# Kernel optimization log

Measured on AMD Instinct MI355X. Metric: run time of the kernel, lower is better.

Reference implementation:

```python
import jax, jax.numpy as jnp
import numpy as np

B, S, E, H, D = 4, 2048, 1024, 8, 128
EPS = 1e-5


def _ln(x, g, b):
    m = jnp.mean(x, axis=-1, keepdims=True)
    v = jnp.mean((x - m) ** 2, axis=-1, keepdims=True)
    return (x - m) * jax.lax.rsqrt(v + EPS) * g + b


def _xavier(k, shape, fan_in, fan_out):
    lim = float(np.sqrt(6.0 / (fan_in + fan_out)))
    return jax.random.uniform(k, shape, jnp.float32, -lim, lim)


def setup_inputs() -> dict:
    key = jax.random.key(0)
    ks = jax.random.split(key, 10)
    return {
        "x": jax.random.normal(ks[0], (B, S, E), jnp.float32),
        # embedding_to_z: Linear(E, H*D); stored as [E, H*D] for x @ W
        "W_ez": _xavier(ks[1], (E, H * D), E, H * D),
        "b_ez": jnp.zeros((H * D,), jnp.float32),
        "U_h": _xavier(ks[2], (H, D, D), D, D),
        "U_z": _xavier(ks[3], (H, D, D), D, D),
        "b_u": jnp.zeros((H, D), jnp.float32),
        "out_shaper": _xavier(ks[4], (H, D, D), D, D),
        # shared per-step state LayerNorm
        "lns_g": jnp.ones((D,), jnp.float32),
        "lns_b": jnp.zeros((D,), jnp.float32),
        # per-head FFN: LayerNorm(D) -> Linear(D,D) -> GELU -> Linear(D,E)
        "ff_ln_g": jnp.ones((H, D), jnp.float32),
        "ff_ln_b": jnp.zeros((H, D), jnp.float32),
        "ff_W1": _xavier(ks[5], (H, D, D), D, D),
        "ff_b1": jnp.zeros((H, D), jnp.float32),
        "ff_W2": _xavier(ks[6], (H, D, E), D, E),
        "ff_b2": jnp.zeros((H, E), jnp.float32),
        # layer_attention_weights: Linear(E, 1)
        "w_att": _xavier(ks[7], (E,), E, 1),
        "b_att": jnp.zeros((), jnp.float32),
        # output LayerNorm
        "lno_g": jnp.ones((E,), jnp.float32),
        "lno_b": jnp.zeros((E,), jnp.float32),
    }


def reference(x, W_ez, b_ez, U_h, U_z, b_u, out_shaper, lns_g, lns_b,
              ff_ln_g, ff_ln_b, ff_W1, ff_b1, ff_W2, ff_b2,
              w_att, b_att, lno_g, lno_b):
    b, s, _ = x.shape
    h, d = U_h.shape[0], U_h.shape[1]
    # z tokens: [B,S,H,D]
    z = jnp.tanh((x @ W_ez + b_ez).reshape(b, s, h, d))
    # torch.einsum('bhd,hdd->bhd') takes the DIAGONAL of the second operand
    uh_diag = jnp.einsum('hii->hi', U_h)          # [H,D]
    uz_diag = jnp.einsum('hii->hi', U_z)          # [H,D]
    os_diag = jnp.einsum('hii->hi', out_shaper)   # [H,D]

    def step(h_prev, z_t):
        # h_prev, z_t: [B,H,D]
        u = jax.nn.sigmoid(h_prev * uh_diag + z_t * uz_diag + b_u)
        h_new = u * h_prev + (1.0 - u) * z_t
        h_new = _ln(h_new, lns_g, lns_b)
        return h_new, h_new

    h0 = jnp.zeros((b, h, d), x.dtype)
    _, states = jax.lax.scan(step, h0, jnp.swapaxes(z, 0, 1))  # [S,B,H,D]
    states = jnp.swapaxes(states, 0, 1)                         # [B,S,H,D]

    shaped = states * os_diag                                   # diag einsum
    hln = _ln(shaped, ff_ln_g, ff_ln_b)                         # per-head LN
    h1 = jax.nn.gelu(jnp.einsum('bshd,hde->bshe', hln, ff_W1) + ff_b1,
                     approximate=False)                         # [B,S,H,D]
    ff_out = jnp.einsum('bshd,hde->bshe', h1, ff_W2) + ff_b2    # [B,S,H,E]

    scores = jax.nn.softmax(jnp.einsum('bshe,e->bsh', ff_out, w_att) + b_att,
                            axis=2)                             # over heads
    weighted = jnp.einsum('bshe,bsh->bse', ff_out, scores)      # [B,S,E]
    return _ln(weighted, lno_g, lno_b)
```

## Files before the change

### kernel.cpp

```cpp
#include <hip/hip_runtime.h>
#include <hip/hip_bf16.h>
#include <math.h>

#define BB 4
#define SS 2048
#define EE 1024
#define HH 8
#define DD 128
#define BSR (BB*SS)
#define HD  (HH*DD)
#define LNEPS 1e-5f
#define LOG2E 1.4426950408889634f

typedef __attribute__((ext_vector_type(8))) short bf16x8;
typedef __attribute__((ext_vector_type(4))) float f32x4;

__device__ __forceinline__ ushort f2bf(float f) {
    union { float f; unsigned u; } c{f};
    unsigned r = c.u + 0x7fff + ((c.u >> 16) & 1);
    return (ushort)(r >> 16);
}
__device__ __forceinline__ float bf2f(ushort b) {
    union { unsigned u; float f; } c{(unsigned)b << 16};
    return c.f;
}

typedef __attribute__((address_space(1))) const unsigned int GUI;
typedef __attribute__((address_space(3))) unsigned int LUI;
__device__ __forceinline__ void gl_lds16(const ushort* g, ushort* l) {
    __builtin_amdgcn_global_load_lds((GUI*)g, (LUI*)l, 16, 0, 0);
}

__device__ __forceinline__ float dpp_add(float x, const int ctrl) {
    int y;
    switch (ctrl) {
        case 0x111: y = __builtin_amdgcn_update_dpp(0, __float_as_int(x), 0x111, 0xf, 0xf, true); break;
        case 0x112: y = __builtin_amdgcn_update_dpp(0, __float_as_int(x), 0x112, 0xf, 0xf, true); break;
        case 0x114: y = __builtin_amdgcn_update_dpp(0, __float_as_int(x), 0x114, 0xf, 0xf, true); break;
        case 0x118: y = __builtin_amdgcn_update_dpp(0, __float_as_int(x), 0x118, 0xf, 0xf, true); break;
        case 0x142: y = __builtin_amdgcn_update_dpp(0, __float_as_int(x), 0x142, 0xf, 0xf, true); break;
        default:    y = __builtin_amdgcn_update_dpp(0, __float_as_int(x), 0x143, 0xf, 0xf, true); break;
    }
    return x + __int_as_float(y);
}

__device__ __forceinline__ float wave_sum64(float x) {
    x = dpp_add(x, 0x111);
    x = dpp_add(x, 0x112);
    x = dpp_add(x, 0x114);
    x = dpp_add(x, 0x118);
    x = dpp_add(x, 0x142);
    x = dpp_add(x, 0x143);
    return __int_as_float(__builtin_amdgcn_readlane(__float_as_int(x), 63));
}

__global__ __launch_bounds__(256)
void convx2_k(const float* __restrict__ x,
              ushort* __restrict__ hi, ushort* __restrict__ lo)
{
    const size_t idx = ((size_t)blockIdx.x * 256 + threadIdx.x) * 4;
    const float4 v = *(const float4*)(x + idx);
    ushort4 oh, ol;
    oh.x = f2bf(v.x); ol.x = f2bf(v.x - bf2f(oh.x));
    oh.y = f2bf(v.y); ol.y = f2bf(v.y - bf2f(oh.y));
    oh.z = f2bf(v.z); ol.z = f2bf(v.z - bf2f(oh.z));
    oh.w = f2bf(v.w); ol.w = f2bf(v.w - bf2f(oh.w));
    *(ushort4*)(hi + idx) = oh;
    *(ushort4*)(lo + idx) = ol;
}

__global__ __launch_bounds__(256)
void prepall_k(const float* __restrict__ W_ez,
               ushort* __restrict__ Wth, ushort* __restrict__ Wtl,
               const float* __restrict__ W2, ushort* __restrict__ W2t,
               const float* __restrict__ W1, ushort* __restrict__ W1t,
               const float* __restrict__ w_att, const float* __restrict__ b2,
               const float* __restrict__ b_att,
               const float* __restrict__ Uh, const float* __restrict__ Uz,
               const float* __restrict__ Os,
               float* __restrict__ q, float* __restrict__ c,
               float* __restrict__ uh_d, float* __restrict__ uz_d,
               float* __restrict__ os_d)
{
    __shared__ float tile[32][33];
    const int blk = blockIdx.x;
    const int tx = threadIdx.x & 31, ty = threadIdx.x >> 5;
    if (blk < 1024) {
        const int k0 = (blk >> 5) * 32, n0 = (blk & 31) * 32;
        #pragma unroll
        for (int i = 0; i < 4; ++i)
            tile[ty + i*8][tx] = W_ez[(size_t)(k0 + ty + i*8) * 1024 + n0 + tx];
        __syncthreads();
        #pragma unroll
        for (int i = 0; i < 4; ++i) {
            const float v = tile[tx][ty + i*8];
            const ushort h = f2bf(v);
            Wth[(size_t)(n0 + ty + i*8) * 1024 + k0 + tx] = h;
            Wtl[(size_t)(n0 + ty + i*8) * 1024 + k0 + tx] = f2bf(v - bf2f(h));
        }
    } else if (blk < 2048) {
        const int b2i = blk - 1024;
        const int k0 = (b2i >> 5) * 32, n0 = (b2i & 31) * 32;
        #pragma unroll
        for (int i = 0; i < 4; ++i)
            tile[ty + i*8][tx] = W2[(size_t)(k0 + ty + i*8) * 1024 + n0 + tx];
        __syncthreads();
        #pragma unroll
        for (int i = 0; i < 4; ++i)
            W2t[(size_t)(n0 + ty + i*8) * 1024 + k0 + tx] = f2bf(tile[tx][ty + i*8]);
    } else if (blk < 2176) {
        const int idx = blk - 2048;
        const int hh = idx >> 4;
        const int k0 = (idx & 3) * 32, n0 = ((idx >> 2) & 3) * 32;
        const float* Wb = W1 + (size_t)hh * DD * DD;
        ushort*      Wtb = W1t + (size_t)hh * DD * DD;
        #pragma unroll
        for (int i = 0; i < 4; ++i)
            tile[ty + i*8][tx] = Wb[(size_t)(k0 + ty + i*8) * DD + n0 + tx];
        __syncthreads();
        #pragma unroll
        for (int i = 0; i < 4; ++i)
            Wtb[(size_t)(n0 + ty + i*8) * DD + k0 + tx] = f2bf(tile[tx][ty + i*8]);
    } else {
        const int gid  = (blk - 2176) * 256 + threadIdx.x;
        const int wave = gid >> 6, lane = gid & 63;
        if (wave < HD) {
            const float* wp = W2 + (size_t)wave * EE;
            float p = 0.f;
            for (int e = lane; e < EE; e += 64) p = fmaf(wp[e], w_att[e], p);
            #pragma unroll
            for (int off = 32; off > 0; off >>= 1) p += __shfl_xor(p, off, 64);
            if (lane == 0) {
                q[wave] = p;
                const int h = wave >> 7, d = wave & 127;
                uh_d[wave] = Uh[(size_t)h*DD*DD + (size_t)d*DD + d];
                uz_d[wave] = Uz[(size_t)h*DD*DD + (size_t)d*DD + d];
                os_d[wave] = Os[(size_t)h*DD*DD + (size_t)d*DD + d];
            }
        } else if (wave < HD + HH) {
            const int h = wave - HD;
            const float* bp = b2 + (size_t)h * EE;
            float p = 0.f;
            for (int e = lane; e < EE; e += 64) p = fmaf(bp[e], w_att[e], p);
            #pragma unroll
            for (int off = 32; off > 0; off >>= 1) p += __shfl_xor(p, off, 64);
            if (lane == 0) c[h] = p + b_att[0];
        }
    }
}

__global__ __launch_bounds__(256)
void gemm_mfma_hp(const ushort* __restrict__ Ah, const ushort* __restrict__ Al,
                  const ushort* __restrict__ Bh, const ushort* __restrict__ Bl,
                  float* __restrict__ C, const float* __restrict__ bias)
{
    __shared__ ushort AsmH[128*32], AsmL[128*32];
    __shared__ ushort BsmH[128*32], BsmL[128*32];
    const int t = threadIdx.x, lane = t & 63, w = t >> 6;
    const int wr = w >> 1, wc = w & 1;
    const int row0 = blockIdx.x * 128, col0 = blockIdx.y * 128;

    const int lr = lane >> 2;
    const int lc = (lane & 3) ^ (lr & 3);
    const size_t aoff0 = (size_t)(row0 +      w*16 + lr) * 1024 + lc*8;
    const size_t aoff1 = (size_t)(row0 + 64 + w*16 + lr) * 1024 + lc*8;
    const size_t boff0 = (size_t)(col0 +      w*16 + lr) * 1024 + lc*8;
    const size_t boff1 = (size_t)(col0 + 64 + w*16 + lr) * 1024 + lc*8;
    ushort* AH0 = AsmH + (     w*16) * 32;  ushort* AH1 = AsmH + (64 + w*16) * 32;
    ushort* AL0 = AsmL + (     w*16) * 32;  ushort* AL1 = AsmL + (64 + w*16) * 32;
    ushort* BH0 = BsmH + (     w*16) * 32;  ushort* BH1 = BsmH + (64 + w*16) * 32;
    ushort* BL0 = BsmL + (     w*16) * 32;  ushort* BL1 = BsmL + (64 + w*16) * 32;

    f32x4 acc[4][4];
    #pragma unroll
    for (int i = 0; i < 4; ++i)
        #pragma unroll
        for (int j = 0; j < 4; ++j) acc[i][j] = (f32x4){0.f,0.f,0.f,0.f};

    const int quad = lane >> 4;
    const int fr   = lane & 15;
    const int fchk = (quad ^ (lane & 3)) * 8;

    for (int k0 = 0; k0 < 1024; k0 += 32) {
        __syncthreads();
        gl_lds16(Ah + aoff0 + k0, AH0);
        gl_lds16(Ah + aoff1 + k0, AH1);
        gl_lds16(Bh + boff0 + k0, BH0);
        gl_lds16(Bh + boff1 + k0, BH1);
        gl_lds16(Al + aoff0 + k0, AL0);
        gl_lds16(Al + aoff1 + k0, AL1);
        gl_lds16(Bl + boff0 + k0, BL0);
        gl_lds16(Bl + boff1 + k0, BL1);
        __syncthreads();

        bf16x8 afh[4], afl[4], bfh[4], bfl[4];
        #pragma unroll
        for (int i = 0; i < 4; ++i) {
            const int ra = (wr*64 + i*16 + fr) * 32 + fchk;
            afh[i] = *(const bf16x8*)(AsmH + ra);
            afl[i] = *(const bf16x8*)(AsmL + ra);
            const int rb = (wc*64 + i*16 + fr) * 32 + fchk;
            bfh[i] = *(const bf16x8*)(BsmH + rb);
            bfl[i] = *(const bf16x8*)(BsmL + rb);
        }
        #pragma unroll
        for (int i = 0; i < 4; ++i)
            #pragma unroll
            for (int j = 0; j < 4; ++j) {
                acc[i][j] = __builtin_amdgcn_mfma_f32_16x16x32_bf16(
                    afh[i], bfl[j], acc[i][j], 0, 0, 0);
                acc[i][j] = __builtin_amdgcn_mfma_f32_16x16x32_bf16(
                    afl[i], bfh[j], acc[i][j], 0, 0, 0);
                acc[i][j] = __builtin_amdgcn_mfma_f32_16x16x32_bf16(
                    afh[i], bfh[j], acc[i][j], 0, 0, 0);
            }
    }

    float colv[4];
    #pragma unroll
    for (int tj = 0; tj < 4; ++tj)
        colv[tj] = bias[col0 + wc*64 + tj*16 + fr];
    #pragma unroll
    for (int ti = 0; ti < 4; ++ti)
        #pragma unroll
        for (int i = 0; i < 4; ++i) {
            const int row = row0 + wr*64 + ti*16 + quad*4 + i;
            #pragma unroll
            for (int tj = 0; tj < 4; ++tj) {
                const int col = col0 + wc*64 + tj*16 + fr;
                C[(size_t)row*1024 + col] = tanhf(acc[ti][tj][i] + colv[tj]);
            }
        }
}

__global__ __launch_bounds__(256)
void gemm_mfma(const ushort* __restrict__ A, const ushort* __restrict__ Bt,
               float* __restrict__ C,
               const float* __restrict__ scores, const float* __restrict__ b2)
{
    __shared__ ushort Asm[128*32];
    __shared__ ushort Bsm[128*32];
    const int t = threadIdx.x, lane = t & 63, w = t >> 6;
    const int wr = w >> 1, wc = w & 1;
    const int row0 = blockIdx.x * 128, col0 = blockIdx.y * 128;

    const int lr = lane >> 2;
    const int lc = (lane & 3) ^ (lr & 3);
    const ushort* Ag0 = A  + (size_t)(row0 +      w*16 + lr) * 1024 + lc*8;
    const ushort* Ag1 = A  + (size_t)(row0 + 64 + w*16 + lr) * 1024 + lc*8;
    const ushort* Bg0 = Bt + (size_t)(col0 +      w*16 + lr) * 1024 + lc*8;
    const ushort* Bg1 = Bt + (size_t)(col0 + 64 + w*16 + lr) * 1024 + lc*8;
    ushort* Al0 = Asm + (     w*16) * 32;
    ushort* Al1 = Asm + (64 + w*16) * 32;
    ushort* Bl0 = Bsm + (     w*16) * 32;
    ushort* Bl1 = Bsm + (64 + w*16) * 32;

    f32x4 acc[4][4];
    #pragma unroll
    for (int i = 0; i < 4; ++i)
        #pragma unroll
        for (int j = 0; j < 4; ++j) acc[i][j] = (f32x4){0.f,0.f,0.f,0.f};

    const int quad = lane >> 4;
    const int fr   = lane & 15;
    const int fchk = (quad ^ (lane & 3)) * 8;

    for (int k0 = 0; k0 < 1024; k0 += 32) {
        __syncthreads();
        gl_lds16(Ag0 + k0, Al0);
        gl_lds16(Ag1 + k0, Al1);
        gl_lds16(Bg0 + k0, Bl0);
        gl_lds16(Bg1 + k0, Bl1);
        __syncthreads();

        bf16x8 af[4], bf[4];
        #pragma unroll
        for (int i = 0; i < 4; ++i) {
            af[i] = *(const bf16x8*)(Asm + (wr*64 + i*16 + fr)*32 + fchk);
            bf[i] = *(const bf16x8*)(Bsm + (wc*64 + i*16 + fr)*32 + fchk);
        }
        #pragma unroll
        for (int i = 0; i < 4; ++i)
            #pragma unroll
            for (int j = 0; j < 4; ++j)
                acc[i][j] = __builtin_amdgcn_mfma_f32_16x16x32_bf16(
                    af[i], bf[j], acc[i][j], 0, 0, 0);
    }

    float b2v[4][HH];
    #pragma unroll
    for (int tj = 0; tj < 4; ++tj) {
        const int col = col0 + wc*64 + tj*16 + fr;
        #pragma unroll
        for (int h = 0; h < HH; ++h) b2v[tj][h] = b2[(size_t)h*EE + col];
    }
    #pragma unroll
    for (int ti = 0; ti < 4; ++ti)
        #pragma unroll
        for (int i = 0; i < 4; ++i) {
            const int row = row0 + wr*64 + ti*16 + quad*4 + i;
            float sc[HH];
            #pragma unroll
            for (int h = 0; h < HH; ++h) sc[h] = scores[row*HH + h];
            #pragma unroll
            for (int tj = 0; tj < 4; ++tj) {
                const int col = col0 + wc*64 + tj*16 + fr;
                float bb = 0.f;
                #pragma unroll
                for (int h = 0; h < HH; ++h) bb = fmaf(sc[h], b2v[tj][h], bb);
                C[(size_t)row*1024 + col] = acc[ti][tj][i] + bb;
            }
        }
}

__global__ __launch_bounds__(256)
void gemm_h1(const ushort* __restrict__ A, const ushort* __restrict__ Bt,
             const float* __restrict__ b1,
             const float* __restrict__ qv, const float* __restrict__ cv,
             ushort* __restrict__ h1b, float* __restrict__ logits)
{
    const int hh = blockIdx.z;
    __shared__ ushort Asm[128*32];
    __shared__ ushort Bsm[128*32];
    __shared__ float lpart[128][2];
    const int t = threadIdx.x, lane = t & 63, w = t >> 6;
    const int wr = w >> 1, wc = w & 1;
    const int row0 = blockIdx.x * 128;

    const int lr = lane >> 2;
    const int lc = (lane & 3) ^ (lr & 3);
    const ushort* Ag0 = A + (size_t)(row0 +      w*16 + lr) * 1024 + hh*DD + lc*8;
    const ushort* Ag1 = A + (size_t)(row0 + 64 + w*16 + lr) * 1024 + hh*DD + lc*8;
    const ushort* Bg0 = Bt + (size_t)hh*DD*DD + (     w*16 + lr) * DD + lc*8;
    const ushort* Bg1 = Bt + (size_t)hh*DD*DD + (64 + w*16 + lr) * DD + lc*8;
    ushort* Al0 = Asm + (     w*16) * 32;
    ushort* Al1 = Asm + (64 + w*16) * 32;
    ushort* Bl0 = Bsm + (     w*16) * 32;
    ushort* Bl1 = Bsm + (64 + w*16) * 32;

    f32x4 acc[4][4];
    #pragma unroll
    for (int i = 0; i < 4; ++i)
        #pragma unroll
        for (int j = 0; j < 4; ++j) acc[i][j] = (f32x4){0.f,0.f,0.f,0.f};

    const int quad = lane >> 4;
    const int fr   = lane & 15;
    const int fchk = (quad ^ (lane & 3)) * 8;

    for (int k0 = 0; k0 < 128; k0 += 32) {
        __syncthreads();
        gl_lds16(Ag0 + k0, Al0);
        gl_lds16(Ag1 + k0, Al1);
        gl_lds16(Bg0 + k0, Bl0);
        gl_lds16(Bg1 + k0, Bl1);
        __syncthreads();

        bf16x8 af[4], bf[4];
        #pragma unroll
        for (int i = 0; i < 4; ++i) {
            af[i] = *(const bf16x8*)(Asm + (wr*64 + i*16 + fr)*32 + fchk);
            bf[i] = *(const bf16x8*)(Bsm + (wc*64 + i*16 + fr)*32 + fchk);
        }
        #pragma unroll
        for (int i = 0; i < 4; ++i)
            #pragma unroll
            for (int j = 0; j < 4; ++j)
                acc[i][j] = __builtin_amdgcn_mfma_f32_16x16x32_bf16(
                    af[i], bf[j], acc[i][j], 0, 0, 0);
    }

    float colv[4], qh[4];
    #pragma unroll
    for (int tj = 0; tj < 4; ++tj) {
        const int col = wc*64 + tj*16 + fr;
        colv[tj] = b1[hh*DD + col];
        qh[tj]   = qv[hh*DD + col];
    }
    #pragma unroll
    for (int ti = 0; ti < 4; ++ti)
        #pragma unroll
        for (int i = 0; i < 4; ++i) {
            const int row = row0 + wr*64 + ti*16 + quad*4 + i;
            float p = 0.f;
            #pragma unroll
            for (int tj = 0; tj < 4; ++tj) {
                const int col = wc*64 + tj*16 + fr;
                float v = acc[ti][tj][i] + colv[tj];
                v = 0.5f * v * (1.f + erff(v * 0.70710678118654752f));
                h1b[(size_t)row*1024 + hh*DD + col] = f2bf(v);
                p = fmaf(v, qh[tj], p);
            }
            p = dpp_add(p, 0x111);
            p = dpp_add(p, 0x112);
            p = dpp_add(p, 0x114);
            p = dpp_add(p, 0x118);
            if (fr == 15)
                lpart[wr*64 + ti*16 + quad*4 + i][wc] = p;
        }
    __syncthreads();
    if (t < 128)
        logits[(size_t)(row0 + t)*HH + hh] = lpart[t][0] + lpart[t][1] + cv[hh];
}

__global__ __launch_bounds__(64)
void scan_k(const float* __restrict__ z,
            const float* __restrict__ uh_d, const float* __restrict__ uz_d,
            const float* __restrict__ b_u,
            const float* __restrict__ lns_g, const float* __restrict__ lns_b,
            ushort* __restrict__ states)
{
    const int bh = blockIdx.x;
    const int b = bh >> 3, h = bh & 7;
    const int l = threadIdx.x;
    const int d0 = 2*l, d1 = d0 + 1;

    const float uhn0 = -uh_d[h*DD+d0] * LOG2E, uhn1 = -uh_d[h*DD+d1] * LOG2E;
    const float uzn0 = -uz_d[h*DD+d0] * LOG2E, uzn1 = -uz_d[h*DD+d1] * LOG2E;
    const float bun0 = -b_u [h*DD+d0] * LOG2E, bun1 = -b_u [h*DD+d1] * LOG2E;
    const float g0  = lns_g[d0], g1 = lns_g[d1];
    const float be0 = lns_b[d0], be1 = lns_b[d1];
    const float A0 = g0 * uhn0, A1 = g1 * uhn1;
    const float bunB0 = fmaf(be0, uhn0, bun0);
    const float bunB1 = fmaf(be1, uhn1, bun1);

    const float* zp = z + ((size_t)b * SS * HH + h) * DD + d0;
    unsigned* op = (unsigned*)(states + (size_t)b * SS * HD + h * DD) + l;

    const int CH = 8;
    float2 zc[CH], zn[CH];
    float pb0[CH], pb1[CH];
    #pragma unroll
    for (int i = 0; i < CH; ++i) zc[i] = *(const float2*)(zp + (size_t)i*HD);
    #pragma unroll
    for (int i = 0; i < CH; ++i) {
        pb0[i] = fmaf(zc[i].x, uzn0, bunB0);
        pb1[i] = fmaf(zc[i].y, uzn1, bunB1);
    }

    float r_c, wp0, wp1, W0, W1, dv0, dv1;

#define PACK_STORE(HP0, HP1, OFF) do {                                       \
        const unsigned pu0 = __float_as_uint(HP0) + 0x8000u;                 \
        const unsigned pu1 = __float_as_uint(HP1) + 0x8000u;                 \
        op[(size_t)(OFF) * (HD/2)] =                                         \
            __builtin_amdgcn_perm(pu1, pu0, 0x07060302u);                    \
    } while (0)

#define SCAN_STEP(ZX, ZY, PB0v, PB1v, ZNX, ZNY, OFF) do {                    \
        const float t0 = fmaf(r_c, W0, (PB0v));                              \
        const float t1 = fmaf(r_c, W1, (PB1v));                              \
        const float e0 = __builtin_amdgcn_exp2f(t0);                         \
        const float e1 = __builtin_amdgcn_exp2f(t1);                         \
        const float u0 = __builtin_amdgcn_rcpf(1.f + e0);                    \
        const float u1 = __builtin_amdgcn_rcpf(1.f + e1);                    \
        const float hn0 = fmaf(u0, dv0, (ZX));                               \
        const float hn1 = fmaf(u1, dv1, (ZY));                               \
        const float s1 = wave_sum64(hn0 + hn1);                              \
        const float s2 = wave_sum64(fmaf(hn0, hn0, hn1*hn1));                \
        const float m   = s1 * (1.f/128.f);                                  \
        const float var = fmaf(s2, 1.f/128.f, -m*m);                         \
        r_c = __builtin_amdgcn_rsqf(var + LNEPS);                            \
        wp0 = hn0 - m; wp1 = hn1 - m;                                        \
        W0 = wp0 * A0; W1 = wp1 * A1;                                        \
        const float hp0 = fmaf(wp0, r_c * g0, be0);                          \
        const float hp1 = fmaf(wp1, r_c * g1, be1);                          \
        PACK_STORE(hp0, hp1, OFF);                                           \
        dv0 = hp0 - (ZNX); dv1 = hp1 - (ZNY);                                \
    } while (0)

    {
        const float z0 = zc[0].x, z1 = zc[0].y;
        const float t0 = fmaf(z0, uzn0, bun0);
        const float t1 = fmaf(z1, uzn1, bun1);
        const float e0 = __builtin_amdgcn_exp2f(t0);
        const float e1 = __builtin_amdgcn_exp2f(t1);
        const float u0 = __builtin_amdgcn_rcpf(1.f + e0);
        const float u1 = __builtin_amdgcn_rcpf(1.f + e1);
        const float hn0 = fmaf(u0, -z0, z0);
        const float hn1 = fmaf(u1, -z1, z1);
        const float s1 = wave_sum64(hn0 + hn1);
        const float s2 = wave_sum64(fmaf(hn0, hn0, hn1*hn1));
        const float m   = s1 * (1.f/128.f);
        const float var = fmaf(s2, 1.f/128.f, -m*m);
        r_c = __builtin_amdgcn_rsqf(var + LNEPS);
        wp0 = hn0 - m; wp1 = hn1 - m;
        W0 = wp0 * A0; W1 = wp1 * A1;
        const float hp0 = fmaf(wp0, r_c * g0, be0);
        const float hp1 = fmaf(wp1, r_c * g1, be1);
        PACK_STORE(hp0, hp1, 0);
        dv0 = hp0 - zc[1].x; dv1 = hp1 - zc[1].y;
    }

    #pragma unroll
    for (int i = 0; i < CH; ++i)
        zn[i] = *(const float2*)(zp + (size_t)(CH+i)*HD);
    #pragma unroll
    for (int i = 1; i < CH; ++i) {
        const float znx = (i+1 < CH) ? zc[i+1].x : zn[0].x;
        const float zny = (i+1 < CH) ? zc[i+1].y : zn[0].y;
        SCAN_STEP(zc[i].x, zc[i].y, pb0[i], pb1[i], znx, zny, i);
    }
    #pragma unroll
    for (int i = 0; i < CH; ++i) {
        zc[i] = zn[i];
        pb0[i] = fmaf(zn[i].x, uzn0, bunB0);
        pb1[i] = fmaf(zn[i].y, uzn1, bunB1);
    }

    for (int s0 = CH; s0 < SS; s0 += CH) {
        if (s0 + CH < SS) {
            #pragma unroll
            for (int i = 0; i < CH; ++i)
                zn[i] = *(const float2*)(zp + (size_t)(s0+CH+i)*HD);
        } else {
            #pragma unroll
            for (int i = 0; i < CH; ++i) zn[i] = make_float2(0.f, 0.f);
        }
        #pragma unroll
        for (int i = 0; i < CH; ++i) {
            const float znx = (i+1 < CH) ? zc[i+1].x : zn[0].x;
            const float zny = (i+1 < CH) ? zc[i+1].y : zn[0].y;
            SCAN_STEP(zc[i].x, zc[i].y, pb0[i], pb1[i], znx, zny, s0 + i);
        }
        #pragma unroll
        for (int i = 0; i < CH; ++i) {
            zc[i] = zn[i];
            pb0[i] = fmaf(zn[i].x, uzn0, bunB0);
            pb1[i] = fmaf(zn[i].y, uzn1, bunB1);
        }
    }
#undef SCAN_STEP
#undef PACK_STORE
}

__global__ __launch_bounds__(256)
void headln_k(const unsigned* __restrict__ st, const float* __restrict__ os_d,
              const float* __restrict__ ffg, const float* __restrict__ ffb,
              unsigned* __restrict__ hln)
{
    const int gid  = blockIdx.x * 256 + threadIdx.x;
    const int row  = gid >> 6;
    const int l    = gid & 63;
    const int h = row & 7;
    const int d0 = 2*l, d1 = d0 + 1;
    const unsigned v = st[(size_t)row * 64 + l];
    const float x0 = bf2f((ushort)(v & 0xffff)) * os_d[h*DD + d0];
    const float x1 = bf2f((ushort)(v >> 16))    * os_d[h*DD + d1];
    float s1 = x0 + x1;
    float s2 = fmaf(x0, x0, x1*x1);
    #pragma unroll
    for (int off = 32; off > 0; off >>= 1) {
        s1 += __shfl_xor(s1, off, 64);
        s2 += __shfl_xor(s2, off, 64);
    }
    const float m   = s1 * (1.f/128.f);
    const float var = fmaf(s2, 1.f/128.f, -m*m);
    const float r   = rsqrtf(var + LNEPS);
    const float o0 = fmaf((x0 - m)*r, ffg[h*DD + d0], ffb[h*DD + d0]);
    const float o1 = fmaf((x1 - m)*r, ffg[h*DD + d1], ffb[h*DD + d1]);
    hln[(size_t)row * 64 + l] = (unsigned)f2bf(o0) | ((unsigned)f2bf(o1) << 16);
}

__global__ __launch_bounds__(256)
void softscale_k(const ushort* __restrict__ h1b, const float* __restrict__ logits,
                 ushort* __restrict__ gb, float* __restrict__ scores)
{
    const int gid = blockIdx.x * 256 + threadIdx.x;
    const size_t idx = (size_t)gid * 4;
    const int bs = (int)(idx >> 10);
    const int h  = (int)((idx >> 7) & 7);
    float l[8];
    float mx = -1e30f;
    #pragma unroll
    for (int i = 0; i < 8; ++i) { l[i] = logits[bs*8 + i]; mx = fmaxf(mx, l[i]); }
    float den = 0.f;
    #pragma unroll
    for (int i = 0; i < 8; ++i) den += __expf(l[i] - mx);
    const float sc = __expf(l[h] - mx) / den;
    const ushort4 v = *(const ushort4*)(h1b + idx);
    ushort4 o;
    o.x = f2bf(bf2f(v.x) * sc); o.y = f2bf(bf2f(v.y) * sc);
    o.z = f2bf(bf2f(v.z) * sc); o.w = f2bf(bf2f(v.w) * sc);
    *(ushort4*)(gb + idx) = o;
    if ((idx & 127) == 0) scores[bs*8 + h] = sc;
}

__global__ __launch_bounds__(256)
void finalln_k(const float* __restrict__ w, const float* __restrict__ g,
               const float* __restrict__ b, float* __restrict__ out)
{
    const int row = blockIdx.x;
    const int t = threadIdx.x;
    const float* xp = w + (size_t)row * EE;
    const float4 v = *(const float4*)(xp + t*4);
    float s1 = v.x + v.y + v.z + v.w;
    float s2 = v.x*v.x + v.y*v.y + v.z*v.z + v.w*v.w;
    #pragma unroll
    for (int off = 32; off > 0; off >>= 1) {
        s1 += __shfl_xor(s1, off, 64);
        s2 += __shfl_xor(s2, off, 64);
    }
    __shared__ float r1[4], r2[4];
    if ((t & 63) == 0) { r1[t>>6] = s1; r2[t>>6] = s2; }
    __syncthreads();
    s1 = r1[0] + r1[1] + r1[2] + r1[3];
    s2 = r2[0] + r2[1] + r2[2] + r2[3];
    const float m   = s1 * (1.f/1024.f);
    const float var = fmaf(s2, 1.f/1024.f, -m*m);
    const float r   = rsqrtf(var + LNEPS);
    const float4 gv = *(const float4*)(g + t*4);
    const float4 bv = *(const float4*)(b + t*4);
    float4 o;
    o.x = fmaf((v.x - m)*r, gv.x, bv.x);
    o.y = fmaf((v.y - m)*r, gv.y, bv.y);
    o.z = fmaf((v.z - m)*r, gv.z, bv.z);
    o.w = fmaf((v.w - m)*r, gv.w, bv.w);
    *(float4*)(out + (size_t)row*EE + t*4) = o;
}

extern "C" void kernel_launch(void* const* d_in, const int* in_sizes, int n_in,
                              void* d_out, int out_size, void* d_ws, size_t ws_size,
                              hipStream_t stream)
{
    const float* x       = (const float*)d_in[0];
    const float* W_ez    = (const float*)d_in[1];
    const float* b_ez    = (const float*)d_in[2];
    const float* U_h     = (const float*)d_in[3];
    const float* U_z     = (const float*)d_in[4];
    const float* b_u     = (const float*)d_in[5];
    const float* outsh   = (const float*)d_in[6];
    const float* lns_g   = (const float*)d_in[7];
    const float* lns_b   = (const float*)d_in[8];
    const float* ff_ln_g = (const float*)d_in[9];
    const float* ff_ln_b = (const float*)d_in[10];
    const float* ff_W1   = (const float*)d_in[11];
    const float* ff_b1   = (const float*)d_in[12];
    const float* ff_W2   = (const float*)d_in[13];
    const float* ff_b2   = (const float*)d_in[14];
    const float* w_att   = (const float*)d_in[15];
    const float* b_att   = (const float*)d_in[16];
    const float* lno_g   = (const float*)d_in[17];
    const float* lno_b   = (const float*)d_in[18];
    float* out = (float*)d_out;

    float* ws = (float*)d_ws;
    const size_t NBIG = (size_t)BSR * HD;
    float* bufA = ws;
    float* bufB = ws + NBIG;
    float* bufC = ws + 2*NBIG;
    float* ext  = ws + 3*NBIG;
    ushort* W2t   = (ushort*)ext;
    ushort* W1t   = (ushort*)(ext + 512*1024);
    float* logits = ext + 512*1024 + 64*1024;
    float* scores = logits + BSR*HH;
    float* qv     = scores + BSR*HH;
    float* cv     = qv + HD;
    float* uh_d   = cv + 8;
    float* uz_d   = uh_d + HD;
    float* os_d   = uz_d + HD;
    ushort* xb_hi = (ushort*)bufB;
    ushort* xb_lo = (ushort*)bufB + NBIG;
    ushort* stb   = (ushort*)bufB;
    ushort* hlnb  = (ushort*)bufB + NBIG;
    float*  wsum  = bufB;
    ushort* WezT_hi = (ushort*)bufC;
    ushort* WezT_lo = (ushort*)bufC + 1024*1024;
    ushort* h1b   = (ushort*)bufC;
    ushort* gb    = (ushort*)bufA;

    convx2_k<<<(BSR*EE/4)/256, 256, 0, stream>>>(x, xb_hi, xb_lo);
    prepall_k<<<2434, 256, 0, stream>>>(W_ez, WezT_hi, WezT_lo,
                                        ff_W2, W2t, ff_W1, W1t,
                                        w_att, ff_b2, b_att,
                                        U_h, U_z, outsh,
                                        qv, cv, uh_d, uz_d, os_d);
    gemm_mfma_hp<<<dim3(64, 8), 256, 0, stream>>>(
        xb_hi, xb_lo, WezT_hi, WezT_lo, bufA, b_ez);
    scan_k<<<BB*HH, 64, 0, stream>>>(bufA, uh_d, uz_d, b_u, lns_g, lns_b, stb);
    headln_k<<<(BSR*HH*64)/256, 256, 0, stream>>>(
        (const unsigned*)stb, os_d, ff_ln_g, ff_ln_b, (unsigned*)hlnb);
    gemm_h1<<<dim3(64, 1, 8), 256, 0, stream>>>(hlnb, W1t, ff_b1, qv, cv,
                                                h1b, logits);
    softscale_k<<<(BSR*HD/4)/256, 256, 0, stream>>>(h1b, logits, gb, scores);
    gemm_mfma<<<dim3(64, 8), 256, 0, stream>>>(gb, W2t, wsum, scores, ff_b2);
    finalln_k<<<BSR, 256, 0, stream>>>(wsum, lno_g, lno_b, out);
}
```

Baseline: 569.4 us.

## Fuse post-scan stages into persistent pipelined kernel overlapping with sequential scan

Replaces the separate scan, head-LN, W1 GEMM, softmax-scale, W2 GEMM and final LN launches with one persistent kernel. 32 blocks run the recurrent scan while 512 worker blocks process sequence chunks of 128 steps as they finish, synchronised through global atomic flag counters. Downstream work can then overlap the long serial scan instead of waiting for it. It adds spin-wait and fence costs, reuses workspace slots in a ring, and risks deadlock if the scan blocks are not co-resident with the spinning workers.

Measured after the change: 1.672 ms. 2.94x slower.

```diff
diff --git a/kernel.cpp b/kernel.cpp
--- a/kernel.cpp
+++ b/kernel.cpp
@@ -11,6 +11,13 @@
 #define HD  (HH*DD)
 #define LNEPS 1e-5f
 #define LOG2E 1.4426950408889634f
+
+#define NCHUNK 16
+#define CHS    128
+#define TPC    160
+#define NTICK  (NCHUNK*TPC)
+#define NWORKER 512
+#define SLOTF  (BB*CHS*1024)
 
 typedef __attribute__((ext_vector_type(8))) short bf16x8;
 typedef __attribute__((ext_vector_type(4))) float f32x4;
@@ -52,6 +59,20 @@
     x = dpp_add(x, 0x142);
     x = dpp_add(x, 0x143);
     return __int_as_float(__builtin_amdgcn_readlane(__float_as_int(x), 63));
+}
+
+__device__ __forceinline__ void wait_ge(unsigned* f, unsigned tgt) {
+    if (threadIdx.x == 0) {
+        while (__hip_atomic_load(f, __ATOMIC_ACQUIRE, __HIP_MEMORY_SCOPE_AGENT) < tgt)
+            __builtin_amdgcn_s_sleep(16);
+    }
+    __syncthreads();
+}
+__device__ __forceinline__ void done_inc(unsigned* f) {
+    __threadfence();
+    __syncthreads();
+    if (threadIdx.x == 0)
+        __hip_atomic_fetch_add(f, 1u, __ATOMIC_RELEASE, __HIP_MEMORY_SCOPE_AGENT);
 }
 
 __global__ __launch_bounds__(256)
@@ -80,10 +101,14 @@
                const float* __restrict__ Os,
                float* __restrict__ q, float* __restrict__ c,
                float* __restrict__ uh_d, float* __restrict__ uz_d,
-               float* __restrict__ os_d)
+               float* __restrict__ os_d, unsigned* __restrict__ flags)
 {
     __shared__ float tile[32][33];
     const int blk = blockIdx.x;
+    if (blk == 2434) {
+        if (threadIdx.x < 128) flags[threadIdx.x] = 0;
+        return;
+    }
     const int tx = threadIdx.x & 31, ty = threadIdx.x >> 5;
     if (blk < 1024) {
         const int k0 = (blk >> 5) * 32, n0 = (blk & 31) * 32;
@@ -234,294 +259,117 @@
 }
 
 __global__ __launch_bounds__(256)
-void gemm_mfma(const ushort* __restrict__ A, const ushort* __restrict__ Bt,
-               float* __restrict__ C,
-               const float* __restrict__ scores, const float* __restrict__ b2)
+void pipeline_k(const float* __restrict__ z,
+                const float* __restrict__ uh_d, const float* __restrict__ uz_d,
+                const float* __restrict__ b_u,
+                const float* __restrict__ lns_g, const float* __restrict__ lns_b,
+                ushort* stb,
+                const float* __restrict__ os_d,
+                const float* __restrict__ ffg, const float* __restrict__ ffb,
+                ushort* __restrict__ hlnb,
+                const ushort* __restrict__ W1t, const float* __restrict__ ff_b1,
+                const float* __restrict__ qv, const float* __restrict__ cv,
+                ushort* __restrict__ h1b, float* __restrict__ logits,
+                ushort* gb,
+                float* __restrict__ scores,
+                const ushort* __restrict__ W2t, const float* __restrict__ ff_b2,
+                float* __restrict__ wslots,
+                const float* __restrict__ lno_g, const float* __restrict__ lno_b,
+                float* __restrict__ out,
+                unsigned* __restrict__ flags)
 {
-    __shared__ ushort Asm[128*32];
-    __shared__ ushort Bsm[128*32];
-    const int t = threadIdx.x, lane = t & 63, w = t >> 6;
-    const int wr = w >> 1, wc = w & 1;
-    const int row0 = blockIdx.x * 128, col0 = blockIdx.y * 128;
-
-    const int lr = lane >> 2;
-    const int lc = (lane & 3) ^ (lr & 3);
-    const ushort* Ag0 = A  + (size_t)(row0 +      w*16 + lr) * 1024 + lc*8;
-    const ushort* Ag1 = A  + (size_t)(row0 + 64 + w*16 + lr) * 1024 + lc*8;
-    const ushort* Bg0 = Bt + (size_t)(col0 +      w*16 + lr) * 1024 + lc*8;
-    const ushort* Bg1 = Bt + (size_t)(col0 + 64 + w*16 + lr) * 1024 + lc*8;
-    ushort* Al0 = Asm + (     w*16) * 32;
-    ushort* Al1 = Asm + (64 + w*16) * 32;
-    ushort* Bl0 = Bsm + (     w*16) * 32;
-    ushort* Bl1 = Bsm + (64 + w*16) * 32;
-
-    f32x4 acc[4][4];
-    #pragma unroll
-    for (int i = 0; i < 4; ++i)
-        #pragma unroll
-        for (int j = 0; j < 4; ++j) acc[i][j] = (f32x4){0.f,0.f,0.f,0.f};
-
-    const int quad = lane >> 4;
-    const int fr   = lane & 15;
-    const int fchk = (quad ^ (lane & 3)) * 8;
-
-    for (int k0 = 0; k0 < 1024; k0 += 32) {
-        __syncthreads();
-        gl_lds16(Ag0 + k0, Al0);
-        gl_lds16(Ag1 + k0, Al1);
-        gl_lds16(Bg0 + k0, Bl0);
-        gl_lds16(Bg1 + k0, Bl1);
-        __syncthreads();
-
-        bf16x8 af[4], bf[4];
-        #pragma unroll
-        for (int i = 0; i < 4; ++i) {
-            af[i] = *(const bf16x8*)(Asm + (wr*64 + i*16 + fr)*32 + fchk);
-            bf[i] = *(const bf16x8*)(Bsm + (wc*64 + i*16 + fr)*32 + fchk);
-        }
-        #pragma unroll
-        for (int i = 0; i < 4; ++i)
-            #pragma unroll
-            for (int j = 0; j < 4; ++j)
-                acc[i][j] = __builtin_amdgcn_mfma_f32_16x16x32_bf16(
-                    af[i], bf[j], acc[i][j], 0, 0, 0);
-    }
-
-    float b2v[4][HH];
-    #pragma unroll
-    for (int tj = 0; tj < 4; ++tj) {
-        const int col = col0 + wc*64 + tj*16 + fr;
-        #pragma unroll
-        for (int h = 0; h < HH; ++h) b2v[tj][h] = b2[(size_t)h*EE + col];
-    }
-    #pragma unroll
-    for (int ti = 0; ti < 4; ++ti)
-        #pragma unroll
-        for (int i = 0; i < 4; ++i) {
-            const int row = row0 + wr*64 + ti*16 + quad*4 + i;
-            float sc[HH];
-            #pragma unroll
-            for (int h = 0; h < HH; ++h) sc[h] = scores[row*HH + h];
-            #pragma unroll
-            for (int tj = 0; tj < 4; ++tj) {
-                const int col = col0 + wc*64 + tj*16 + fr;
-                float bb = 0.f;
-                #pragma unroll
-                for (int h = 0; h < HH; ++h) bb = fmaf(sc[h], b2v[tj][h], bb);
-                C[(size_t)row*1024 + col] = acc[ti][tj][i] + bb;
-            }
-        }
-}
-
-__global__ __launch_bounds__(256)
-void gemm_h1(const ushort* __restrict__ A, const ushort* __restrict__ Bt,
-             const float* __restrict__ b1,
-             const float* __restrict__ qv, const float* __restrict__ cv,
-             ushort* __restrict__ h1b, float* __restrict__ logits)
-{
-    const int hh = blockIdx.z;
-    __shared__ ushort Asm[128*32];
-    __shared__ ushort Bsm[128*32];
-    __shared__ float lpart[128][2];
-    const int t = threadIdx.x, lane = t & 63, w = t >> 6;
-    const int wr = w >> 1, wc = w & 1;
-    const int row0 = blockIdx.x * 128;
-
-    const int lr = lane >> 2;
-    const int lc = (lane & 3) ^ (lr & 3);
-    const ushort* Ag0 = A + (size_t)(row0 +      w*16 + lr) * 1024 + hh*DD + lc*8;
-    const ushort* Ag1 = A + (size_t)(row0 + 64 + w*16 + lr) * 1024 + hh*DD + lc*8;
-    const ushort* Bg0 = Bt + (size_t)hh*DD*DD + (     w*16 + lr) * DD + lc*8;
-    const ushort* Bg1 = Bt + (size_t)hh*DD*DD + (64 + w*16 + lr) * DD + lc*8;
-    ushort* Al0 = Asm + (     w*16) * 32;
-    ushort* Al1 = Asm + (64 + w*16) * 32;
-    ushort* Bl0 = Bsm + (     w*16) * 32;
-    ushort* Bl1 = Bsm + (64 + w*16) * 32;
-
-    f32x4 acc[4][4];
-    #pragma unroll
-    for (int i = 0; i < 4; ++i)
-        #pragma unroll
-        for (int j = 0; j < 4; ++j) acc[i][j] = (f32x4){0.f,0.f,0.f,0.f};
-
-    const int quad = lane >> 4;
-    const int fr   = lane & 15;
-    const int fchk = (quad ^ (lane & 3)) * 8;
-
-    for (int k0 = 0; k0 < 128; k0 += 32) {
-        __syncthreads();
-        gl_lds16(Ag0 + k0, Al0);
-        gl_lds16(Ag1 + k0, Al1);
-        gl_lds16(Bg0 + k0, Bl0);
-        gl_lds16(Bg1 + k0, Bl1);
-        __syncthreads();
-
-        bf16x8 af[4], bf[4];
-        #pragma unroll
-        for (int i = 0; i < 4; ++i) {
-            af[i] = *(const bf16x8*)(Asm + (wr*64 + i*16 + fr)*32 + fchk);
-            bf[i] = *(const bf16x8*)(Bsm + (wc*64 + i*16 + fr)*32 + fchk);
-        }
-        #pragma unroll
-        for (int i = 0; i < 4; ++i)
-            #pragma unroll
-            for (int j = 0; j < 4; ++j)
-                acc[i][j] = __builtin_amdgcn_mfma_f32_16x16x32_bf16(
-                    af[i], bf[j], acc[i][j], 0, 0, 0);
-    }
-
-    float colv[4], qh[4];
-    #pragma unroll
-    for (int tj = 0; tj < 4; ++tj) {
-        const int col = wc*64 + tj*16 + fr;
-        colv[tj] = b1[hh*DD + col];
-        qh[tj]   = qv[hh*DD + col];
-    }
-    #pragma unroll
-    for (int ti = 0; ti < 4; ++ti)
-        #pragma unroll
-        for (int i = 0; i < 4; ++i) {
-            const int row = row0 + wr*64 + ti*16 + quad*4 + i;
-            float p = 0.f;
-            #pragma unroll
-            for (int tj = 0; tj < 4; ++tj) {
-                const int col = wc*64 + tj*16 + fr;
-                float v = acc[ti][tj][i] + colv[tj];
-                v = 0.5f * v * (1.f + erff(v * 0.70710678118654752f));
-                h1b[(size_t)row*1024 + hh*DD + col] = f2bf(v);
-                p = fmaf(v, qh[tj], p);
-            }
-            p = dpp_add(p, 0x111);
-            p = dpp_add(p, 0x112);
-            p = dpp_add(p, 0x114);
-            p = dpp_add(p, 0x118);
-            if (fr == 15)
-                lpart[wr*64 + ti*16 + quad*4 + i][wc] = p;
-        }
-    __syncthreads();
-    if (t < 128)
-        logits[(size_t)(row0 + t)*HH + hh] = lpart[t][0] + lpart[t][1] + cv[hh];
-}
-
-__global__ __launch_bounds__(64)
-void scan_k(const float* __restrict__ z,
-            const float* __restrict__ uh_d, const float* __restrict__ uz_d,
-            const float* __restrict__ b_u,
-            const float* __restrict__ lns_g, const float* __restrict__ lns_b,
-            ushort* __restrict__ states)
-{
-    const int bh = blockIdx.x;
-    const int b = bh >> 3, h = bh & 7;
-    const int l = threadIdx.x;
-    const int d0 = 2*l, d1 = d0 + 1;
-
-    const float uhn0 = -uh_d[h*DD+d0] * LOG2E, uhn1 = -uh_d[h*DD+d1] * LOG2E;
-    const float uzn0 = -uz_d[h*DD+d0] * LOG2E, uzn1 = -uz_d[h*DD+d1] * LOG2E;
-    const float bun0 = -b_u [h*DD+d0] * LOG2E, bun1 = -b_u [h*DD+d1] * LOG2E;
-    const float g0  = lns_g[d0], g1 = lns_g[d1];
-    const float be0 = lns_b[d0], be1 = lns_b[d1];
-    const float A0 = g0 * uhn0, A1 = g1 * uhn1;
-    const float bunB0 = fmaf(be0, uhn0, bun0);
-    const float bunB1 = fmaf(be1, uhn1, bun1);
-
-    const float* zp = z + ((size_t)b * SS * HH + h) * DD + d0;
-    unsigned* op = (unsigned*)(states + (size_t)b * SS * HD + h * DD) + l;
-
-    const int CH = 8;
-    float2 zc[CH], zn[CH];
-    float pb0[CH], pb1[CH];
-    #pragma unroll
-    for (int i = 0; i < CH; ++i) zc[i] = *(const float2*)(zp + (size_t)i*HD);
-    #pragma unroll
-    for (int i = 0; i < CH; ++i) {
-        pb0[i] = fmaf(zc[i].x, uzn0, bunB0);
-        pb1[i] = fmaf(zc[i].y, uzn1, bunB1);
-    }
-
-    float r_c, wp0, wp1, W0, W1, dv0, dv1;
+    if (blockIdx.x < 32) {
+        if (threadIdx.x >= 64) return;
+        const int bh = blockIdx.x;
+        const int b = bh >> 3, h = bh & 7;
+        const int l = threadIdx.x;
+        const int d0 = 2*l, d1 = d0 + 1;
+
+        const float uhn0 = -uh_d[h*DD+d0] * LOG2E, uhn1 = -uh_d[h*DD+d1] * LOG2E;
+        const float uzn0 = -uz_d[h*DD+d0] * LOG2E, uzn1 = -uz_d[h*DD+d1] * LOG2E;
+        const float bun0 = -b_u [h*DD+d0] * LOG2E, bun1 = -b_u [h*DD+d1] * LOG2E;
+        const float g0  = lns_g[d0], g1 = lns_g[d1];
+        const float be0 = lns_b[d0], be1 = lns_b[d1];
+        const float A0 = g0 * uhn0, A1 = g1 * uhn1;
+        const float bunB0 = fmaf(be0, uhn0, bun0);
+        const float bunB1 = fmaf(be1, uhn1, bun1);
+
+        const float* zp = z + ((size_t)b * SS * HH + h) * DD + d0;
+        unsigned* op = (unsigned*)(stb + (size_t)b * SS * HD + h * DD) + l;
+
+        const int CH = 8;
+        float2 zc[CH], zn[CH];
+        float pb0[CH], pb1[CH];
+        #pragma unroll
+        for (int i = 0; i < CH; ++i) zc[i] = *(const float2*)(zp + (size_t)i*HD);
+        #pragma unroll
+        for (int i = 0; i < CH; ++i) {
+            pb0[i] = fmaf(zc[i].x, uzn0, bunB0);
+            pb1[i] = fmaf(zc[i].y, uzn1, bunB1);
+        }
+
+        float r_c, wp0, wp1, W0, W1, dv0, dv1;
 
 #define PACK_STORE(HP0, HP1, OFF) do {                                       \
-        const unsigned pu0 = __float_as_uint(HP0) + 0x8000u;                 \
-        const unsigned pu1 = __float_as_uint(HP1) + 0x8000u;                 \
-        op[(size_t)(OFF) * (HD/2)] =                                         \
-            __builtin_amdgcn_perm(pu1, pu0, 0x07060302u);                    \
-    } while (0)
+            const unsigned pu0 = __float_as_uint(HP0) + 0x8000u;             \
+            const unsigned pu1 = __float_as_uint(HP1) + 0x8000u;             \
+            op[(size_t)(OFF) * (HD/2)] =                                     \
+                __builtin_amdgcn_perm(pu1, pu0, 0x07060302u);                \
+        } while (0)
 
 #define SCAN_STEP(ZX, ZY, PB0v, PB1v, ZNX, ZNY, OFF) do {                    \
-        const float t0 = fmaf(r_c, W0, (PB0v));                              \
-        const float t1 = fmaf(r_c, W1, (PB1v));                              \
-        const float e0 = __builtin_amdgcn_exp2f(t0);                         \
-        const float e1 = __builtin_amdgcn_exp2f(t1);                         \
-        const float u0 = __builtin_amdgcn_rcpf(1.f + e0);                    \
-        const float u1 = __builtin_amdgcn_rcpf(1.f + e1);                    \
-        const float hn0 = fmaf(u0, dv0, (ZX));                               \
-        const float hn1 = fmaf(u1, dv1, (ZY));                               \
-        const float s1 = wave_sum64(hn0 + hn1);                              \
-        const float s2 = wave_sum64(fmaf(hn0, hn0, hn1*hn1));                \
-        const float m   = s1 * (1.f/128.f);                                  \
-        const float var = fmaf(s2, 1.f/128.f, -m*m);                         \
-        r_c = __builtin_amdgcn_rsqf(var + LNEPS);                            \
-        wp0 = hn0 - m; wp1 = hn1 - m;                                        \
-        W0 = wp0 * A0; W1 = wp1 * A1;                                        \
-        const float hp0 = fmaf(wp0, r_c * g0, be0);                          \
-        const float hp1 = fmaf(wp1, r_c * g1, be1);                          \
-        PACK_STORE(hp0, hp1, OFF);                                           \
-        dv0 = hp0 - (ZNX); dv1 = hp1 - (ZNY);                                \
-    } while (0)
-
-    {
-        const float z0 = zc[0].x, z1 = zc[0].y;
-        const float t0 = fmaf(z0, uzn0, bun0);
-        const float t1 = fmaf(z1, uzn1, bun1);
-        const float e0 = __builtin_amdgcn_exp2f(t0);
-        const float e1 = __builtin_amdgcn_exp2f(t1);
-        const float u0 = __builtin_amdgcn_rcpf(1.f + e0);
-        const float u1 = __builtin_amdgcn_rcpf(1.f + e1);
-        const float hn0 = fmaf(u0, -z0, z0);
-        const float hn1 = fmaf(u1, -z1, z1);
-        const float s1 = wave_sum64(hn0 + hn1);
-        const float s2 = wave_sum64(fmaf(hn0, hn0, hn1*hn1));
-        const float m   = s1 * (1.f/128.f);
-        const float var = fmaf(s2, 1.f/128.f, -m*m);
-        r_c = __builtin_amdgcn_rsqf(var + LNEPS);
-        wp0 = hn0 - m; wp1 = hn1 - m;
-        W0 = wp0 * A0; W1 = wp1 * A1;
-        const float hp0 = fmaf(wp0, r_c * g0, be0);
-        const float hp1 = fmaf(wp1, r_c * g1, be1);
-        PACK_STORE(hp0, hp1, 0);
-        dv0 = hp0 - zc[1].x; dv1 = hp1 - zc[1].y;
-    }
-
-    #pragma unroll
-    for (int i = 0; i < CH; ++i)
-        zn[i] = *(const float2*)(zp + (size_t)(CH+i)*HD);
-    #pragma unroll
-    for (int i = 1; i < CH; ++i) {
-        const float znx = (i+1 < CH) ? zc[i+1].x : zn[0].x;
-        const float zny = (i+1 < CH) ? zc[i+1].y : zn[0].y;
-        SCAN_STEP(zc[i].x, zc[i].y, pb0[i], pb1[i], znx, zny, i);
-    }
-    #pragma unroll
-    for (int i = 0; i < CH; ++i) {
-        zc[i] = zn[i];
-        pb0[i] = fmaf(zn[i].x, uzn0, bunB0);
-        pb1[i] = fmaf(zn[i].y, uzn1, bunB1);
-    }
-
-    for (int s0 = CH; s0 < SS; s0 += CH) {
-        if (s0 + CH < SS) {
-            #pragma unroll
-            for (int i = 0; i < CH; ++i)
-                zn[i] = *(const float2*)(zp + (size_t)(s0+CH+i)*HD);
-        } else {
-            #pragma unroll
-            for (int i = 0; i < CH; ++i) zn[i] = make_float2(0.f, 0.f);
-        }
-        #pragma unroll
-        for (int i = 0; i < CH; ++i) {
+            const float t0 = fmaf(r_c, W0, (PB0v));                          \
+            const float t1 = fmaf(r_c, W1, (PB1v));                          \
+            const float e0 = __builtin_amdgcn_exp2f(t0);                     \
+            const float e1 = __builtin_amdgcn_exp2f(t1);                     \
+            const float u0 = __builtin_amdgcn_rcpf(1.f + e0);                \
+            const float u1 = __builtin_amdgcn_rcpf(1.f + e1);                \
+            const float hn0 = fmaf(u0, dv0, (ZX));                           \
+            const float hn1 = fmaf(u1, dv1, (ZY));                           \
+            const float s1 = wave_sum64(hn0 + hn1);                          \
+            const float s2 = wave_sum64(fmaf(hn0, hn0, hn1*hn1));            \
+            const float m   = s1 * (1.f/128.f);                              \
+            const float var = fmaf(s2, 1.f/128.f, -m*m);                     \
+            r_c = __builtin_amdgcn_rsqf(var + LNEPS);                        \
+            wp0 = hn0 - m; wp1 = hn1 - m;                                    \
+            W0 = wp0 * A0; W1 = wp1 * A1;                                    \
+            const float hp0 = fmaf(wp0, r_c * g0, be0);                      \
+            const float hp1 = fmaf(wp1, r_c * g1, be1);                      \
+            PACK_STORE(hp0, hp1, OFF);                                       \
+            dv0 = hp0 - (ZNX); dv1 = hp1 - (ZNY);                            \
+        } while (0)
+
+        {
+            const float z0 = zc[0].x, z1 = zc[0].y;
+            const float t0 = fmaf(z0, uzn0, bun0);
+            const float t1 = fmaf(z1, uzn1, bun1);
+            const float e0 = __builtin_amdgcn_exp2f(t0);
+            const float e1 = __builtin_amdgcn_exp2f(t1);
+            const float u0 = __builtin_amdgcn_rcpf(1.f + e0);
+            const float u1 = __builtin_amdgcn_rcpf(1.f + e1);
+            const float hn0 = fmaf(u0, -z0, z0);
+            const float hn1 = fmaf(u1, -z1, z1);
+            const float s1 = wave_sum64(hn0 + hn1);
+            const float s2 = wave_sum64(fmaf(hn0, hn0, hn1*hn1));
+            const float m   = s1 * (1.f/128.f);
+            const float var = fmaf(s2, 1.f/128.f, -m*m);
+            r_c = __builtin_amdgcn_rsqf(var + LNEPS);
+            wp0 = hn0 - m; wp1 = hn1 - m;
+            W0 = wp0 * A0; W1 = wp1 * A1;
+            const float hp0 = fmaf(wp0, r_c * g0, be0);
+            const float hp1 = fmaf(wp1, r_c * g1, be1);
+            PACK_STORE(hp0, hp1, 0);
+            dv0 = hp0 - zc[1].x; dv1 = hp1 - zc[1].y;
+        }
+
+        #pragma unroll
+        for (int i = 0; i < CH; ++i)
+            zn[i] = *(const float2*)(zp + (size_t)(CH+i)*HD);
+        #pragma unroll
+        for (int i = 1; i < CH; ++i) {
             const float znx = (i+1 < CH) ? zc[i+1].x : zn[0].x;
             const float zny = (i+1 < CH) ? zc[i+1].y : zn[0].y;
-            SCAN_STEP(zc[i].x, zc[i].y, pb0[i], pb1[i], znx, zny, s0 + i);
+            SCAN_STEP(zc[i].x, zc[i].y, pb0[i], pb1[i], znx, zny, i);
         }
         #pragma unroll
         for (int i = 0; i < CH; ++i) {
@@ -529,94 +377,309 @@
             pb0[i] = fmaf(zn[i].x, uzn0, bunB0);
             pb1[i] = fmaf(zn[i].y, uzn1, bunB1);
         }
-    }
+
+        for (int s0 = CH; s0 < SS; s0 += CH) {
+            if (s0 + CH < SS) {
+                #pragma unroll
+                for (int i = 0; i < CH; ++i)
+                    zn[i] = *(const float2*)(zp + (size_t)(s0+CH+i)*HD);
+            } else {
+                #pragma unroll
+                for (int i = 0; i < CH; ++i) zn[i] = make_float2(0.f, 0.f);
+            }
+            #pragma unroll
+            for (int i = 0; i < CH; ++i) {
+                const float znx = (i+1 < CH) ? zc[i+1].x : zn[0].x;
+                const float zny = (i+1 < CH) ? zc[i+1].y : zn[0].y;
+                SCAN_STEP(zc[i].x, zc[i].y, pb0[i], pb1[i], znx, zny, s0 + i);
+            }
+            #pragma unroll
+            for (int i = 0; i < CH; ++i) {
+                zc[i] = zn[i];
+                pb0[i] = fmaf(zn[i].x, uzn0, bunB0);
+                pb1[i] = fmaf(zn[i].y, uzn1, bunB1);
+            }
+            if ((s0 & (CHS-1)) == CHS - CH) {
+                __threadfence();
+                if (threadIdx.x == 0)
+                    __hip_atomic_fetch_add(&flags[1 + (s0 >> 7)], 1u,
+                                           __ATOMIC_RELEASE, __HIP_MEMORY_SCOPE_AGENT);
+            }
+        }
 #undef SCAN_STEP
 #undef PACK_STORE
-}
-
-__global__ __launch_bounds__(256)
-void headln_k(const unsigned* __restrict__ st, const float* __restrict__ os_d,
-              const float* __restrict__ ffg, const float* __restrict__ ffb,
-              unsigned* __restrict__ hln)
-{
-    const int gid  = blockIdx.x * 256 + threadIdx.x;
-    const int row  = gid >> 6;
-    const int l    = gid & 63;
-    const int h = row & 7;
-    const int d0 = 2*l, d1 = d0 + 1;
-    const unsigned v = st[(size_t)row * 64 + l];
-    const float x0 = bf2f((ushort)(v & 0xffff)) * os_d[h*DD + d0];
-    const float x1 = bf2f((ushort)(v >> 16))    * os_d[h*DD + d1];
-    float s1 = x0 + x1;
-    float s2 = fmaf(x0, x0, x1*x1);
-    #pragma unroll
-    for (int off = 32; off > 0; off >>= 1) {
-        s1 += __shfl_xor(s1, off, 64);
-        s2 += __shfl_xor(s2, off, 64);
+        return;
     }
-    const float m   = s1 * (1.f/128.f);
-    const float var = fmaf(s2, 1.f/128.f, -m*m);
-    const float r   = rsqrtf(var + LNEPS);
-    const float o0 = fmaf((x0 - m)*r, ffg[h*DD + d0], ffb[h*DD + d0]);
-    const float o1 = fmaf((x1 - m)*r, ffg[h*DD + d1], ffb[h*DD + d1]);
-    hln[(size_t)row * 64 + l] = (unsigned)f2bf(o0) | ((unsigned)f2bf(o1) << 16);
-}
-
-__global__ __launch_bounds__(256)
-void softscale_k(const ushort* __restrict__ h1b, const float* __restrict__ logits,
-                 ushort* __restrict__ gb, float* __restrict__ scores)
-{
-    const int gid = blockIdx.x * 256 + threadIdx.x;
-    const size_t idx = (size_t)gid * 4;
-    const int bs = (int)(idx >> 10);
-    const int h  = (int)((idx >> 7) & 7);
-    float l[8];
-    float mx = -1e30f;
-    #pragma unroll
-    for (int i = 0; i < 8; ++i) { l[i] = logits[bs*8 + i]; mx = fmaxf(mx, l[i]); }
-    float den = 0.f;
-    #pragma unroll
-    for (int i = 0; i < 8; ++i) den += __expf(l[i] - mx);
-    const float sc = __expf(l[h] - mx) / den;
-    const ushort4 v = *(const ushort4*)(h1b + idx);
-    ushort4 o;
-    o.x = f2bf(bf2f(v.x) * sc); o.y = f2bf(bf2f(v.y) * sc);
-    o.z = f2bf(bf2f(v.z) * sc); o.w = f2bf(bf2f(v.w) * sc);
-    *(ushort4*)(gb + idx) = o;
-    if ((idx & 127) == 0) scores[bs*8 + h] = sc;
-}
-
-__global__ __launch_bounds__(256)
-void finalln_k(const float* __restrict__ w, const float* __restrict__ g,
-               const float* __restrict__ b, float* __restrict__ out)
-{
-    const int row = blockIdx.x;
-    const int t = threadIdx.x;
-    const float* xp = w + (size_t)row * EE;
-    const float4 v = *(const float4*)(xp + t*4);
-    float s1 = v.x + v.y + v.z + v.w;
-    float s2 = v.x*v.x + v.y*v.y + v.z*v.z + v.w*v.w;
-    #pragma unroll
-    for (int off = 32; off > 0; off >>= 1) {
-        s1 += __shfl_xor(s1, off, 64);
-        s2 += __shfl_xor(s2, off, 64);
+
+    __shared__ ushort Asm[128*32];
+    __shared__ ushort Bsm[128*32];
+    __shared__ float lpart[128][2];
+    __shared__ float r1s[4], r2s[4];
+    __shared__ unsigned s_tk;
+    const int tid = threadIdx.x;
+
+    for (;;) {
+        __syncthreads();
+        if (tid == 0) s_tk = atomicAdd(&flags[0], 1u);
+        __syncthreads();
+        const unsigned tk = s_tk;
+        if (tk >= NTICK) return;
+        const int c  = (int)(tk / TPC);
+        const int r  = (int)(tk % TPC);
+
+        if (r < 32) {
+            wait_ge(&flags[1 + c], 32);
+            const int b = r >> 3, i8 = r & 7;
+            const int bs0 = b*SS + c*CHS + i8*16;
+            const int l = tid & 63;
+            const int d0 = 2*l, d1 = d0 + 1;
+            const unsigned* st_u = (const unsigned*)stb;
+            unsigned* hln_u = (unsigned*)hlnb;
+            for (int it = 0; it < 32; ++it) {
+                const int u  = it*4 + (tid >> 6);
+                const int bs = bs0 + (u >> 3);
+                const int h  = u & 7;
+                const int row = bs*8 + h;
+                const unsigned v = st_u[(size_t)row*64 + l];
+                const float x0 = bf2f((ushort)(v & 0xffff)) * os_d[h*DD + d0];
+                const float x1 = bf2f((ushort)(v >> 16))    * os_d[h*DD + d1];
+                float s1 = x0 + x1;
+                float s2 = fmaf(x0, x0, x1*x1);
+                #pragma unroll
+                for (int off = 32; off > 0; off >>= 1) {
+                    s1 += __shfl_xor(s1, off, 64);
+                    s2 += __shfl_xor(s2, off, 64);
+                }
+                const float m   = s1 * (1.f/128.f);
+                const float var = fmaf(s2, 1.f/128.f, -m*m);
+                const float rr  = rsqrtf(var + LNEPS);
+                const float o0 = fmaf((x0 - m)*rr, ffg[h*DD + d0], ffb[h*DD + d0]);
+                const float o1 = fmaf((x1 - m)*rr, ffg[h*DD + d1], ffb[h*DD + d1]);
+                hln_u[(size_t)row*64 + l] = (unsigned)f2bf(o0) | ((unsigned)f2bf(o1) << 16);
+            }
+            done_inc(&flags[17 + c]);
+        } else if (r < 64) {
+            wait_ge(&flags[17 + c], 32);
+            const int sub = r - 32;
+            const int bb = sub >> 3, hh = sub & 7;
+            const int row0 = bb*SS + c*CHS;
+            const int lane = tid & 63, w = tid >> 6;
+            const int wr = w >> 1, wc = w & 1;
+            const int lr = lane >> 2;
+            const int lc = (lane & 3) ^ (lr & 3);
+            const ushort* Ag0 = hlnb + (size_t)(row0 +      w*16 + lr) * 1024 + hh*DD + lc*8;
+            const ushort* Ag1 = hlnb + (size_t)(row0 + 64 + w*16 + lr) * 1024 + hh*DD + lc*8;
+            const ushort* Bg0 = W1t + (size_t)hh*DD*DD + (     w*16 + lr) * DD + lc*8;
+            const ushort* Bg1 = W1t + (size_t)hh*DD*DD + (64 + w*16 + lr) * DD + lc*8;
+            ushort* Al0 = Asm + (     w*16) * 32;
+            ushort* Al1 = Asm + (64 + w*16) * 32;
+            ushort* Bl0 = Bsm + (     w*16) * 32;
+            ushort* Bl1 = Bsm + (64 + w*16) * 32;
+
+            f32x4 acc[4][4];
+            #pragma unroll
+            for (int i = 0; i < 4; ++i)
+                #pragma unroll
+                for (int j = 0; j < 4; ++j) acc[i][j] = (f32x4){0.f,0.f,0.f,0.f};
+
+            const int quad = lane >> 4;
+            const int fr   = lane & 15;
+            const int fchk = (quad ^ (lane & 3)) * 8;
+
+            for (int k0 = 0; k0 < 128; k0 += 32) {
+                __syncthreads();
+                gl_lds16(Ag0 + k0, Al0);
+                gl_lds16(Ag1 + k0, Al1);
+                gl_lds16(Bg0 + k0, Bl0);
+                gl_lds16(Bg1 + k0, Bl1);
+                __syncthreads();
+
+                bf16x8 af[4], bf[4];
+                #pragma unroll
+                for (int i = 0; i < 4; ++i) {
+                    af[i] = *(const bf16x8*)(Asm + (wr*64 + i*16 + fr)*32 + fchk);
+                    bf[i] = *(const bf16x8*)(Bsm + (wc*64 + i*16 + fr)*32 + fchk);
+                }
+                #pragma unroll
+                for (int i = 0; i < 4; ++i)
+                    #pragma unroll
+                    for (int j = 0; j < 4; ++j)
+                        acc[i][j] = __builtin_amdgcn_mfma_f32_16x16x32_bf16(
+                            af[i], bf[j], acc[i][j], 0, 0, 0);
+            }
+
+            float colv[4], qh[4];
+            #pragma unroll
+            for (int tj = 0; tj < 4; ++tj) {
+                const int col = wc*64 + tj*16 + fr;
+                colv[tj] = ff_b1[hh*DD + col];
+                qh[tj]   = qv[hh*DD + col];
+            }
+            #pragma unroll
+            for (int ti = 0; ti < 4; ++ti)
+                #pragma unroll
+                for (int i = 0; i < 4; ++i) {
+                    const int row = row0 + wr*64 + ti*16 + quad*4 + i;
+                    float p = 0.f;
+                    #pragma unroll
+                    for (int tj = 0; tj < 4; ++tj) {
+                        const int col = wc*64 + tj*16 + fr;
+                        float v = acc[ti][tj][i] + colv[tj];
+                        v = 0.5f * v * (1.f + erff(v * 0.70710678118654752f));
+                        h1b[(size_t)row*1024 + hh*DD + col] = f2bf(v);
+                        p = fmaf(v, qh[tj], p);
+                    }
+                    p = dpp_add(p, 0x111);
+                    p = dpp_add(p, 0x112);
+                    p = dpp_add(p, 0x114);
+                    p = dpp_add(p, 0x118);
+                    if (fr == 15)
+                        lpart[wr*64 + ti*16 + quad*4 + i][wc] = p;
+                }
+            __syncthreads();
+            if (tid < 128)
+                logits[(size_t)(row0 + tid)*HH + hh] = lpart[tid][0] + lpart[tid][1] + cv[hh];
+            done_inc(&flags[33 + c]);
+        } else if (r < 96) {
+            wait_ge(&flags[33 + c], 32);
+            const int sub = r - 64;
+            const int b = sub >> 3, i8 = sub & 7;
+            const int bs0 = b*SS + c*CHS + i8*16;
+            const int h = (tid >> 5) & 7;
+            for (int it = 0; it < 16; ++it) {
+                const int bs = bs0 + it;
+                const size_t idx = (size_t)bs*1024 + (size_t)tid*4;
+                float lv[8];
+                float mx = -1e30f;
+                #pragma unroll
+                for (int i = 0; i < 8; ++i) { lv[i] = logits[bs*8 + i]; mx = fmaxf(mx, lv[i]); }
+                float den = 0.f;
+                #pragma unroll
+                for (int i = 0; i < 8; ++i) den += __expf(lv[i] - mx);
+                const float sc = __expf(lv[h] - mx) / den;
+                const ushort4 v = *(const ushort4*)(h1b + idx);
+                ushort4 o;
+                o.x = f2bf(bf2f(v.x) * sc); o.y = f2bf(bf2f(v.y) * sc);
+                o.z = f2bf(bf2f(v.z) * sc); o.w = f2bf(bf2f(v.w) * sc);
+                *(ushort4*)(gb + idx) = o;
+                if ((tid & 31) == 0) scores[bs*8 + h] = sc;
+            }
+            done_inc(&flags[49 + c]);
+        } else if (r < 128) {
+            wait_ge(&flags[49 + c], 32);
+            if (c >= 8) wait_ge(&flags[81 + c - 8], 32);
+            const int sub = r - 96;
+            const int bb = sub >> 3, cb = sub & 7;
+            const int row0 = bb*SS + c*CHS, col0 = cb*128;
+            float* wslot = wslots + (size_t)(c & 7) * SLOTF;
+            const int lane = tid & 63, w = tid >> 6;
+            const int wr = w >> 1, wc = w & 1;
+            const int lr = lane >> 2;
+            const int lc = (lane & 3) ^ (lr & 3);
+            const ushort* Ag0 = gb  + (size_t)(row0 +      w*16 + lr) * 1024 + lc*8;
+            const ushort* Ag1 = gb  + (size_t)(row0 + 64 + w*16 + lr) * 1024 + lc*8;
+            const ushort* Bg0 = W2t + (size_t)(col0 +      w*16 + lr) * 1024 + lc*8;
+            const ushort* Bg1 = W2t + (size_t)(col0 + 64 + w*16 + lr) * 1024 + lc*8;
+            ushort* Al0 = Asm + (     w*16) * 32;
+            ushort* Al1 = Asm + (64 + w*16) * 32;
+            ushort* Bl0 = Bsm + (     w*16) * 32;
+            ushort* Bl1 = Bsm + (64 + w*16) * 32;
+
+            f32x4 acc[4][4];
+            #pragma unroll
+            for (int i = 0; i < 4; ++i)
+                #pragma unroll
+                for (int j = 0; j < 4; ++j) acc[i][j] = (f32x4){0.f,0.f,0.f,0.f};
+
+            const int quad = lane >> 4;
+            const int fr   = lane & 15;
+            const int fchk = (quad ^ (lane & 3)) * 8;
+
+            for (int k0 = 0; k0 < 1024; k0 += 32) {
+                __syncthreads();
+                gl_lds16(Ag0 + k0, Al0);
+                gl_lds16(Ag1 + k0, Al1);
+                gl_lds16(Bg0 + k0, Bl0);
+                gl_lds16(Bg1 + k0, Bl1);
+                __syncthreads();
+
+                bf16x8 af[4], bf[4];
+                #pragma unroll
+                for (int i = 0; i < 4; ++i) {
+                    af[i] = *(const bf16x8*)(Asm + (wr*64 + i*16 + fr)*32 + fchk);
+                    bf[i] = *(const bf16x8*)(Bsm + (wc*64 + i*16 + fr)*32 + fchk);
+                }
+                #pragma unroll
+                for (int i = 0; i < 4; ++i)
+                    #pragma unroll
+                    for (int j = 0; j < 4; ++j)
+                        acc[i][j] = __builtin_amdgcn_mfma_f32_16x16x32_bf16(
+                            af[i], bf[j], acc[i][j], 0, 0, 0);
+            }
+
+            float b2v[4][HH];
+            #pragma unroll
+            for (int tj = 0; tj < 4; ++tj) {
+                const int col = col0 + wc*64 + tj*16 + fr;
+                #pragma unroll
+                for (int h = 0; h < HH; ++h) b2v[tj][h] = ff_b2[(size_t)h*EE + col];
+            }
+            #pragma unroll
+            for (int ti = 0; ti < 4; ++ti)
+                #pragma unroll
+                for (int i = 0; i < 4; ++i) {
+                    const int row  = row0 + wr*64 + ti*16 + quad*4 + i;
+                    const int lrow = bb*128 + wr*64 + ti*16 + quad*4 + i;
+                    float sc[HH];
+                    #pragma unroll
+                    for (int h = 0; h < HH; ++h) sc[h] = scores[row*HH + h];
+                    #pragma unroll
+                    for (int tj = 0; tj < 4; ++tj) {
+                        const int col = col0 + wc*64 + tj*16 + fr;
+                        float bbv = 0.f;
+                        #pragma unroll
+                        for (int h = 0; h < HH; ++h) bbv = fmaf(sc[h], b2v[tj][h], bbv);
+                        wslot[(size_t)lrow*1024 + col] = acc[ti][tj][i] + bbv;
+                    }
+                }
+            done_inc(&flags[65 + c]);
+        } else {
+            wait_ge(&flags[65 + c], 32);
+            const int sub = r - 128;
+            const int b = sub >> 3, i8 = sub & 7;
+            const float* wslot = wslots + (size_t)(c & 7) * SLOTF;
+            const float4 gv = *(const float4*)(lno_g + tid*4);
+            const float4 bv = *(const float4*)(lno_b + tid*4);
+            for (int it = 0; it < 16; ++it) {
+                const int rin  = i8*16 + it;
+                const int lrow = b*128 + rin;
+                const int orow = b*SS + c*CHS + rin;
+                const float4 v = *(const float4*)(wslot + (size_t)lrow*1024 + tid*4);
+                float s1 = v.x + v.y + v.z + v.w;
+                float s2 = v.x*v.x + v.y*v.y + v.z*v.z + v.w*v.w;
+                #pragma unroll
+                for (int off = 32; off > 0; off >>= 1) {
+                    s1 += __shfl_xor(s1, off, 64);
+                    s2 += __shfl_xor(s2, off, 64);
+                }
+                if ((tid & 63) == 0) { r1s[tid>>6] = s1; r2s[tid>>6] = s2; }
+                __syncthreads();
+                s1 = r1s[0] + r1s[1] + r1s[2] + r1s[3];
+                s2 = r2s[0] + r2s[1] + r2s[2] + r2s[3];
+                const float m   = s1 * (1.f/1024.f);
+                const float var = fmaf(s2, 1.f/1024.f, -m*m);
+                const float rr  = rsqrtf(var + LNEPS);
+                float4 o;
+                o.x = fmaf((v.x - m)*rr, gv.x, bv.x);
+                o.y = fmaf((v.y - m)*rr, gv.y, bv.y);
+                o.z = fmaf((v.z - m)*rr, gv.z, bv.z);
+                o.w = fmaf((v.w - m)*rr, gv.w, bv.w);
+                *(float4*)(out + (size_t)orow*EE + tid*4) = o;
+                __syncthreads();
+            }
+            done_inc(&flags[81 + c]);
+        }
     }
-    __shared__ float r1[4], r2[4];
-    if ((t & 63) == 0) { r1[t>>6] = s1; r2[t>>6] = s2; }
-    __syncthreads();
-    s1 = r1[0] + r1[1] + r1[2] + r1[3];
-    s2 = r2[0] + r2[1] + r2[2] + r2[3];
-    const float m   = s1 * (1.f/1024.f);
-    const float var = fmaf(s2, 1.f/1024.f, -m*m);
-    const float r   = rsqrtf(var + LNEPS);
-    const float4 gv = *(const float4*)(g + t*4);
-    const float4 bv = *(const float4*)(b + t*4);
-    float4 o;
-    o.x = fmaf((v.x - m)*r, gv.x, bv.x);
-    o.y = fmaf((v.y - m)*r, gv.y, bv.y);
-    o.z = fmaf((v.z - m)*r, gv.z, bv.z);
-    o.w = fmaf((v.w - m)*r, gv.w, bv.w);
-    *(float4*)(out + (size_t)row*EE + t*4) = o;
 }
 
 extern "C" void kernel_launch(void* const* d_in, const int* in_sizes, int n_in,
@@ -659,30 +722,29 @@
     float* uh_d   = cv + 8;
     float* uz_d   = uh_d + HD;
     float* os_d   = uz_d + HD;
+    unsigned* flags = (unsigned*)(os_d + HD);
     ushort* xb_hi = (ushort*)bufB;
     ushort* xb_lo = (ushort*)bufB + NBIG;
     ushort* stb   = (ushort*)bufB;
     ushort* hlnb  = (ushort*)bufB + NBIG;
-    float*  wsum  = bufB;
     ushort* WezT_hi = (ushort*)bufC;
     ushort* WezT_lo = (ushort*)bufC + 1024*1024;
     ushort* h1b   = (ushort*)bufC;
-    ushort* gb    = (ushort*)bufA;
+    float*  wslots = bufC + 4*1024*1024;
+    ushort* gb    = stb;
 
     convx2_k<<<(BSR*EE/4)/256, 256, 0, stream>>>(x, xb_hi, xb_lo);
-    prepall_k<<<2434, 256, 0, stream>>>(W_ez, WezT_hi, WezT_lo,
+    prepall_k<<<2435, 256, 0, stream>>>(W_ez, WezT_hi, WezT_lo,
                                         ff_W2, W2t, ff_W1, W1t,
                                         w_att, ff_b2, b_att,
                                         U_h, U_z, outsh,
-                                        qv, cv, uh_d, uz_d, os_d);
+                                        qv, cv, uh_d, uz_d, os_d, flags);
     gemm_mfma_hp<<<dim3(64, 8), 256, 0, stream>>>(
         xb_hi, xb_lo, WezT_hi, WezT_lo, bufA, b_ez);
-    scan_k<<<BB*HH, 64, 0, stream>>>(bufA, uh_d, uz_d, b_u, lns_g, lns_b, stb);
-    headln_k<<<(BSR*HH*64)/256, 256, 0, stream>>>(
-        (const unsigned*)stb, os_d, ff_ln_g, ff_ln_b, (unsigned*)hlnb);
-    gemm_h1<<<dim3(64, 1, 8), 256, 0, stream>>>(hlnb, W1t, ff_b1, qv, cv,
-                                                h1b, logits);
-    softscale_k<<<(BSR*HD/4)/256, 256, 0, stream>>>(h1b, logits, gb, scores);
-    gemm_mfma<<<dim3(64, 8), 256, 0, stream>>>(gb, W2t, wsum, scores, ff_b2);
-    finalln_k<<<BSR, 256, 0, stream>>>(wsum, lno_g, lno_b, out);
-}
+    pipeline_k<<<32 + NWORKER, 256, 0, stream>>>(
+        bufA, uh_d, uz_d, b_u, lns_g, lns_b, stb,
+        os_d, ff_ln_g, ff_ln_b, hlnb,
+        W1t, ff_b1, qv, cv, h1b, logits,
+        gb, scores, W2t, ff_b2, wslots,
+        lno_g, lno_b, out, flags);
+}
```
